# Kernel optimization log

Hardware: AMD Instinct MI355X
Metric: run time of the kernel (lower is better)

## Reference

```python
import jax, jax.numpy as jnp
import numpy as np

L = 3          # num_legs
D = 32         # leg_dim == out_leg_dim (output_dim = input_dim = D**L)
NUM_NODES = 6  # num_levels * (num_legs - 1) = 3 * 2
B = 256        # batch


def setup_inputs() -> dict:
    key = jax.random.key(0)
    k1, k2 = jax.random.split(key, 2)
    inputs = jax.random.normal(k1, (B, D ** L), dtype=jnp.float32)
    # all 6 entangler nodes share shape (D,D,D,D) since leg_dim == out_leg_dim;
    # scale ~ 1/D to mimic glorot and keep the 6-contraction chain numerically sane
    nodes = jax.random.normal(k2, (NUM_NODES, D, D, D, D), dtype=jnp.float32) / D
    bias = jnp.zeros((D ** L,), dtype=jnp.float32)
    return {"inputs": inputs, "nodes": nodes, "bias": bias}


def reference(inputs, nodes, bias):
    # Faithful port of DenseEntangler.call: reshape the input vector to L legs,
    # then contract NUM_NODES 4-leg tensors; node i eats edge slots (i%L, (i+1)%L)
    # with its axes (0,1) and replaces them with its axes (2,3).
    # jnp.tensordot output axis order (free axes of x in order, then node axes 2,3)
    # matches tn.contract_between's default ordering, so the final flatten is identical.
    Bn = inputs.shape[0]
    x = inputs.reshape((Bn,) + (D,) * L)   # axis 0 = batch, axes 1..L = legs
    pos = list(range(1, L + 1))            # edge slot k -> current axis of x
    for i in range(NUM_NODES):
        s0, s1 = i % L, (i + 1) % L
        p, q = pos[s0], pos[s1]
        x = jnp.tensordot(x, nodes[i], axes=[[p, q], [0, 1]])
        # remaining axes of x keep order (batch stays axis 0); new node axes go last
        new_pos = [0] * L
        for k in range(L):
            if k == s0:
                new_pos[k] = L - 1
            elif k == s1:
                new_pos[k] = L
            else:
                a = pos[k]
                new_pos[k] = a - (p < a) - (q < a)
        pos = new_pos
    out = x.reshape(Bn, -1) + bias  # flatten in current axis order, as in the TF code
    return jax.nn.relu(out)
```

## Files before the change

### kernel.cpp

```cpp
#include <hip/hip_runtime.h>
#include <hip/hip_bf16.h>
#include <stdint.h>

using bf16 = __hip_bfloat16;
typedef __attribute__((ext_vector_type(8))) short short8;
typedef __attribute__((ext_vector_type(4))) float floatx4;

#define DD 32
#define DL3 32768
#define BATCH 256
#define NK 1024

#define BM 256
#define BN 128
#define NKT 16
#define A_ELEM 16384
#define B_ELEM 8192
#define BUF_ELEM 24576
#define LDS_BYTES 147456

__device__ __forceinline__ void load16(const void* g, void* l) {
  __builtin_amdgcn_global_load_lds((const __attribute__((address_space(1))) void*)g,
                                   (__attribute__((address_space(3))) void*)l,
                                   16, 0, 0);
}

__global__ __launch_bounds__(256) void prep_x(const float* __restrict__ x, bf16* __restrict__ dst) {
  int b = blockIdx.x >> 5, v = blockIdx.x & 31;
  __shared__ float tile[32][33];
  const float* xb = x + (size_t)b * DL3 + v * DD;
  int t = threadIdx.x;
#pragma unroll
  for (int it = 0; it < 4; ++it) {
    int u = (t >> 5) + it * 8, f = t & 31;
    tile[u][f] = xb[u * NK + f];
  }
  __syncthreads();
  bf16* db = dst + (size_t)b * DL3 + v * NK;
#pragma unroll
  for (int it = 0; it < 4; ++it) {
    int f = (t >> 5) + it * 8, u = t & 31;
    db[f * DD + u] = __float2bfloat16(tile[u][f]);
  }
}

__global__ __launch_bounds__(256) void prep_nodes(const float* __restrict__ nodes, bf16* __restrict__ dst) {
  int id = blockIdx.x;
  int nb = id & 31, kb = (id >> 5) & 31, i = id >> 10;
  const float* src = nodes + (size_t)i * 1048576;
  bf16* d = dst + (size_t)i * 1048576;
  __shared__ float tile[32][33];
  int t = threadIdx.x;
#pragma unroll
  for (int it = 0; it < 4; ++it) {
    int u = (t >> 5) + it * 8, j = t & 31;
    tile[u][j] = src[(size_t)(u * 32 + kb) * 1024 + nb * 32 + j];
  }
  __syncthreads();
#pragma unroll
  for (int it = 0; it < 4; ++it) {
    int j = (t >> 5) + it * 8, u = t & 31;
    d[(size_t)(nb * 32 + j) * 1024 + kb * 32 + u] = __float2bfloat16(tile[u][j]);
  }
}

template <bool FINAL>
__global__ __launch_bounds__(512, 2) void entangler_gemm(
    const bf16* __restrict__ A, const bf16* __restrict__ Bn,
    bf16* __restrict__ Cb, float* __restrict__ Cf, const float* __restrict__ bias) {
  extern __shared__ char smem[];
  bf16* lds = (bf16*)smem;

  const int t = threadIdx.x;
  const int lane = t & 63;
  const int lane16 = lane & 15, quad = lane >> 4;
  const int w = t >> 6;
  const int wm = (w >> 2) & 1, wn = (w >> 1) & 1, wk = w & 1;
  const int sel = (lane16 >> 1) & 3;
  const int qs = (quad ^ sel) * 8;
  const int b0 = blockIdx.x * 8;
  const int N0 = blockIdx.y * 128;

  const int aRd = wk * 8192 + (wm * 128 + lane16) * 32 + qs;
  const int bRd = A_ELEM + wk * 4096 + (wn * 64 + lane16) * 32 + qs;

  int aOff[4], aLds[4], bOff[2], bLds[2];
#pragma unroll
  for (int r = 0; r < 4; ++r) {
    int P = (r * 512 + t) * 16;
    int L = P ^ (((P >> 7) & 3) << 4);
    int kk = L >> 14, m = (L >> 6) & 255, u0 = (L & 63) >> 1;
    aOff[r] = (b0 + (m >> 5)) * DL3 + kk * NK + (m & 31) * 32 + u0;
    aLds[r] = P >> 1;
  }
#pragma unroll
  for (int r = 0; r < 2; ++r) {
    int P = (r * 512 + t) * 16;
    int L = P ^ (((P >> 7) & 3) << 4);
    int kk = L >> 13, n = (L >> 6) & 127, u0 = (L & 63) >> 1;
    bOff[r] = (N0 + n) * NK + kk * 32 + u0;
    bLds[r] = A_ELEM + (P >> 1);
  }

  floatx4 acc[8][4];
#pragma unroll
  for (int i = 0; i < 8; ++i)
#pragma unroll
    for (int j = 0; j < 4; ++j)
      acc[i][j] = (floatx4){0.f, 0.f, 0.f, 0.f};

#pragma unroll
  for (int s = 0; s < 2; ++s) {
    bf16* bp = lds + s * BUF_ELEM;
#pragma unroll
    for (int r = 0; r < 4; ++r) load16(A + aOff[r] + s * 2048, bp + aLds[r]);
#pragma unroll
    for (int r = 0; r < 2; ++r) load16(Bn + bOff[r] + s * 64, bp + bLds[r]);
  }
  asm volatile("s_waitcnt vmcnt(6)" ::: "memory");
  __builtin_amdgcn_s_barrier();
  asm volatile("" ::: "memory");

#pragma unroll
  for (int kt = 0; kt < NKT; ++kt) {
    const bf16* bp = lds + (kt % 3) * BUF_ELEM;
    short8 af[8], bfr[4];
#pragma unroll
    for (int i = 0; i < 8; ++i) af[i] = *(const short8*)(bp + aRd + i * 512);
#pragma unroll
    for (int j = 0; j < 4; ++j) bfr[j] = *(const short8*)(bp + bRd + j * 512);
    if (kt < NKT - 2) {
      bf16* np = lds + ((kt + 2) % 3) * BUF_ELEM;
#pragma unroll
      for (int r = 0; r < 4; ++r) load16(A + aOff[r] + (kt + 2) * 2048, np + aLds[r]);
#pragma unroll
      for (int r = 0; r < 2; ++r) load16(Bn + bOff[r] + (kt + 2) * 64, np + bLds[r]);
    }
    asm volatile("" ::: "memory");
    __builtin_amdgcn_s_barrier();
    asm volatile("" ::: "memory");
    __builtin_amdgcn_s_setprio(1);
#pragma unroll
    for (int i = 0; i < 8; ++i)
#pragma unroll
      for (int j = 0; j < 4; ++j)
        acc[i][j] = __builtin_amdgcn_mfma_f32_16x16x32_bf16(af[i], bfr[j], acc[i][j], 0, 0, 0);
    __builtin_amdgcn_s_setprio(0);
    if (kt < NKT - 2) {
      asm volatile("s_waitcnt vmcnt(6)" ::: "memory");
    } else if (kt == NKT - 2) {
      asm volatile("s_waitcnt vmcnt(0)" ::: "memory");
    }
    if (kt < NKT - 1) {
      __builtin_amdgcn_s_barrier();
      asm volatile("" ::: "memory");
    }
  }

  __syncthreads();
  float* red = (float*)smem;
  const int pair = (wm << 1) | wn;
  if (wk == 1) {
    float* dst = red + pair * 8192;
#pragma unroll
    for (int i = 0; i < 8; ++i)
#pragma unroll
      for (int j = 0; j < 4; ++j)
        *(floatx4*)(dst + ((i * 4 + j) * 64 + lane) * 4) = acc[i][j];
  }
  __syncthreads();
  if (wk == 0) {
    const float* src = red + pair * 8192;
    const int R0 = blockIdx.x * 256;
#pragma unroll
    for (int i = 0; i < 8; ++i) {
#pragma unroll
      for (int j = 0; j < 4; ++j) {
        floatx4 p = *(const floatx4*)(src + ((i * 4 + j) * 64 + lane) * 4);
        acc[i][j] += p;
#pragma unroll
        for (int r = 0; r < 4; ++r) {
          int row = R0 + wm * 128 + i * 16 + quad * 4 + r;
          int col = N0 + wn * 64 + j * 16 + lane16;
          if (FINAL) {
            float v = acc[i][j][r] + bias[(row & 31) * 1024 + col];
            Cf[(size_t)row * 1024 + col] = fmaxf(v, 0.f);
          } else {
            Cb[(size_t)row * 1024 + col] = __float2bfloat16(acc[i][j][r]);
          }
        }
      }
    }
  }
}

extern "C" void kernel_launch(void* const* d_in, const int* in_sizes, int n_in,
                              void* d_out, int out_size, void* d_ws, size_t ws_size,
                              hipStream_t stream) {
  const float* x     = (const float*)d_in[0];
  const float* nodes = (const float*)d_in[1];
  const float* bias  = (const float*)d_in[2];
  float* out = (float*)d_out;

  bf16* buf0  = (bf16*)d_ws;
  bf16* buf1  = buf0 + (size_t)BATCH * DL3;
  bf16* nodeT = buf1 + (size_t)BATCH * DL3;

  static bool attr_done = false;
  if (!attr_done) {
    hipFuncSetAttribute((const void*)entangler_gemm<false>,
                        hipFuncAttributeMaxDynamicSharedMemorySize, LDS_BYTES);
    hipFuncSetAttribute((const void*)entangler_gemm<true>,
                        hipFuncAttributeMaxDynamicSharedMemorySize, LDS_BYTES);
    attr_done = true;
  }

  prep_x<<<dim3(BATCH * 32), dim3(256), 0, stream>>>(x, buf0);
  prep_nodes<<<dim3(6 * 1024), dim3(256), 0, stream>>>(nodes, nodeT);

  dim3 grid(32, 8), blk(512);
  entangler_gemm<false><<<grid, blk, LDS_BYTES, stream>>>(buf0, nodeT + (size_t)0 * 1048576, buf1, nullptr, nullptr);
  entangler_gemm<false><<<grid, blk, LDS_BYTES, stream>>>(buf1, nodeT + (size_t)1 * 1048576, buf0, nullptr, nullptr);
  entangler_gemm<false><<<grid, blk, LDS_BYTES, stream>>>(buf0, nodeT + (size_t)2 * 1048576, buf1, nullptr, nullptr);
  entangler_gemm<false><<<grid, blk, LDS_BYTES, stream>>>(buf1, nodeT + (size_t)3 * 1048576, buf0, nullptr, nullptr);
  entangler_gemm<false><<<grid, blk, LDS_BYTES, stream>>>(buf0, nodeT + (size_t)4 * 1048576, buf1, nullptr, nullptr);
  entangler_gemm<true ><<<grid, blk, LDS_BYTES, stream>>>(buf1, nodeT + (size_t)5 * 1048576, nullptr, out, bias);
}
```

Before: 231.2 us.

## Fuse six entangler GEMM launches into one cooperative kernel with grid sync

Replaces the six back-to-back GEMM launches with a single cooperative kernel that loops over the six contraction stages and uses grid.sync between them. This removes per-launch overhead and the tail/ramp gaps between kernels. The K loop is also changed from full unroll to rotating LDS buffer pointers with unroll 1, which shrinks code size but may cost some scheduling freedom. The six-launch path is kept as a fallback if the cooperative launch fails.

```diff
diff --git a/kernel.cpp b/kernel.cpp
--- a/kernel.cpp
+++ b/kernel.cpp
@@ -1,6 +1,9 @@
 #include <hip/hip_runtime.h>
+#include <hip/hip_cooperative_groups.h>
 #include <hip/hip_bf16.h>
 #include <stdint.h>
+
+namespace cg = cooperative_groups;
 
 using bf16 = __hip_bfloat16;
 typedef __attribute__((ext_vector_type(8))) short short8;
@@ -11,11 +14,8 @@
 #define BATCH 256
 #define NK 1024
 
-#define BM 256
-#define BN 128
 #define NKT 16
 #define A_ELEM 16384
-#define B_ELEM 8192
 #define BUF_ELEM 24576
 #define LDS_BYTES 147456
 
@@ -64,13 +64,157 @@
   }
 }
 
+
+__global__ __launch_bounds__(512, 2) void entangler_chain(
+    bf16* __restrict__ buf0, const bf16* __restrict__ nodeT,
+    bf16* __restrict__ buf1, float* __restrict__ out, const float* __restrict__ bias) {
+  extern __shared__ char smem[];
+  bf16* lds = (bf16*)smem;
+
+  const int t = threadIdx.x;
+  const int lane = t & 63;
+  const int lane16 = lane & 15, quad = lane >> 4;
+  const int w = t >> 6;
+  const int wm = (w >> 2) & 1, wn = (w >> 1) & 1, wk = w & 1;
+  const int sel = (lane16 >> 1) & 3;
+  const int qs = (quad ^ sel) * 8;
+  const int xt = blockIdx.x & 31, yt = blockIdx.x >> 5;
+  const int b0 = xt * 8;
+  const int N0 = yt * 128;
+
+  const int aRd = wk * 8192 + (wm * 128 + lane16) * 32 + qs;
+  const int bRd = A_ELEM + wk * 4096 + (wn * 64 + lane16) * 32 + qs;
+
+  int aOff[4], aLds[4], bOff[2], bLds[2];
+#pragma unroll
+  for (int r = 0; r < 4; ++r) {
+    int P = (r * 512 + t) * 16;
+    int L = P ^ (((P >> 7) & 3) << 4);
+    int kk = L >> 14, m = (L >> 6) & 255, u0 = (L & 63) >> 1;
+    aOff[r] = (b0 + (m >> 5)) * DL3 + kk * NK + (m & 31) * 32 + u0;
+    aLds[r] = P >> 1;
+  }
+#pragma unroll
+  for (int r = 0; r < 2; ++r) {
+    int P = (r * 512 + t) * 16;
+    int L = P ^ (((P >> 7) & 3) << 4);
+    int kk = L >> 13, n = (L >> 6) & 127, u0 = (L & 63) >> 1;
+    bOff[r] = (N0 + n) * NK + kk * 32 + u0;
+    bLds[r] = A_ELEM + (P >> 1);
+  }
+
+  cg::grid_group grid = cg::this_grid();
+
+#pragma unroll 1
+  for (int s = 0; s < 6; ++s) {
+    const bf16* Ain = (s & 1) ? buf1 : buf0;
+    bf16* Cw = (s & 1) ? buf0 : buf1;
+    const bf16* Bs = nodeT + (size_t)s * 1048576;
+    const bool FIN = (s == 5);
+
+    floatx4 acc[8][4];
+#pragma unroll
+    for (int i = 0; i < 8; ++i)
+#pragma unroll
+      for (int j = 0; j < 4; ++j)
+        acc[i][j] = (floatx4){0.f, 0.f, 0.f, 0.f};
+
+    bf16* pCur = lds;
+    bf16* pNxt = lds + BUF_ELEM;
+    bf16* pThd = lds + 2 * BUF_ELEM;
+
+#pragma unroll
+    for (int r = 0; r < 4; ++r) load16(Ain + aOff[r], pCur + aLds[r]);
+#pragma unroll
+    for (int r = 0; r < 2; ++r) load16(Bs + bOff[r], pCur + bLds[r]);
+#pragma unroll
+    for (int r = 0; r < 4; ++r) load16(Ain + aOff[r] + 2048, pNxt + aLds[r]);
+#pragma unroll
+    for (int r = 0; r < 2; ++r) load16(Bs + bOff[r] + 64, pNxt + bLds[r]);
+    asm volatile("s_waitcnt vmcnt(6)" ::: "memory");
+    __builtin_amdgcn_s_barrier();
+    asm volatile("" ::: "memory");
+
+#pragma unroll 1
+    for (int kt = 0; kt < NKT; ++kt) {
+      short8 af[8], bfr[4];
+#pragma unroll
+      for (int i = 0; i < 8; ++i) af[i] = *(const short8*)(pCur + aRd + i * 512);
+#pragma unroll
+      for (int j = 0; j < 4; ++j) bfr[j] = *(const short8*)(pCur + bRd + j * 512);
+      if (kt < NKT - 2) {
+#pragma unroll
+        for (int r = 0; r < 4; ++r) load16(Ain + aOff[r] + (kt + 2) * 2048, pThd + aLds[r]);
+#pragma unroll
+        for (int r = 0; r < 2; ++r) load16(Bs + bOff[r] + (kt + 2) * 64, pThd + bLds[r]);
+      }
+      asm volatile("" ::: "memory");
+      __builtin_amdgcn_s_barrier();
+      asm volatile("" ::: "memory");
+      __builtin_amdgcn_s_setprio(1);
+#pragma unroll
+      for (int i = 0; i < 8; ++i)
+#pragma unroll
+        for (int j = 0; j < 4; ++j)
+          acc[i][j] = __builtin_amdgcn_mfma_f32_16x16x32_bf16(af[i], bfr[j], acc[i][j], 0, 0, 0);
+      __builtin_amdgcn_s_setprio(0);
+      if (kt < NKT - 2) {
+        asm volatile("s_waitcnt vmcnt(6)" ::: "memory");
+      } else if (kt == NKT - 2) {
+        asm volatile("s_waitcnt vmcnt(0)" ::: "memory");
+      }
+      if (kt < NKT - 1) {
+        __builtin_amdgcn_s_barrier();
+        asm volatile("" ::: "memory");
+      }
+      bf16* tmp = pCur; pCur = pNxt; pNxt = pThd; pThd = tmp;
+    }
+
+    __syncthreads();
+    float* red = (float*)smem;
+    const int pair = (wm << 1) | wn;
+    if (wk == 1) {
+      float* dst = red + pair * 8192;
+#pragma unroll
+      for (int i = 0; i < 8; ++i)
+#pragma unroll
+        for (int j = 0; j < 4; ++j)
+          *(floatx4*)(dst + ((i * 4 + j) * 64 + lane) * 4) = acc[i][j];
+    }
+    __syncthreads();
+    if (wk == 0) {
+      const float* src = red + pair * 8192;
+      const int R0 = xt * 256;
+#pragma unroll
+      for (int i = 0; i < 8; ++i) {
+#pragma unroll
+        for (int j = 0; j < 4; ++j) {
+          floatx4 p = *(const floatx4*)(src + ((i * 4 + j) * 64 + lane) * 4);
+          acc[i][j] += p;
+#pragma unroll
+          for (int r = 0; r < 4; ++r) {
+            int row = R0 + wm * 128 + i * 16 + quad * 4 + r;
+            int col = N0 + wn * 64 + j * 16 + lane16;
+            if (FIN) {
+              float v = acc[i][j][r] + bias[(row & 31) * 1024 + col];
+              out[(size_t)row * 1024 + col] = fmaxf(v, 0.f);
+            } else {
+              Cw[(size_t)row * 1024 + col] = __float2bfloat16(acc[i][j][r]);
+            }
+          }
+        }
+      }
+    }
+    if (s < 5) grid.sync();
+  }
+}
+
 template <bool FINAL>
 __global__ __launch_bounds__(512, 2) void entangler_gemm(
     const bf16* __restrict__ A, const bf16* __restrict__ Bn,
     bf16* __restrict__ Cb, float* __restrict__ Cf, const float* __restrict__ bias) {
   extern __shared__ char smem[];
   bf16* lds = (bf16*)smem;
-
   const int t = threadIdx.x;
   const int lane = t & 63;
   const int lane16 = lane & 15, quad = lane >> 4;
@@ -80,10 +224,8 @@
   const int qs = (quad ^ sel) * 8;
   const int b0 = blockIdx.x * 8;
   const int N0 = blockIdx.y * 128;
-
   const int aRd = wk * 8192 + (wm * 128 + lane16) * 32 + qs;
   const int bRd = A_ELEM + wk * 4096 + (wn * 64 + lane16) * 32 + qs;
-
   int aOff[4], aLds[4], bOff[2], bLds[2];
 #pragma unroll
   for (int r = 0; r < 4; ++r) {
@@ -101,40 +243,36 @@
     bOff[r] = (N0 + n) * NK + kk * 32 + u0;
     bLds[r] = A_ELEM + (P >> 1);
   }
-
   floatx4 acc[8][4];
 #pragma unroll
   for (int i = 0; i < 8; ++i)
 #pragma unroll
     for (int j = 0; j < 4; ++j)
       acc[i][j] = (floatx4){0.f, 0.f, 0.f, 0.f};
-
-#pragma unroll
-  for (int s = 0; s < 2; ++s) {
-    bf16* bp = lds + s * BUF_ELEM;
-#pragma unroll
-    for (int r = 0; r < 4; ++r) load16(A + aOff[r] + s * 2048, bp + aLds[r]);
-#pragma unroll
-    for (int r = 0; r < 2; ++r) load16(Bn + bOff[r] + s * 64, bp + bLds[r]);
-  }
+  bf16* pCur = lds; bf16* pNxt = lds + BUF_ELEM; bf16* pThd = lds + 2 * BUF_ELEM;
+#pragma unroll
+  for (int r = 0; r < 4; ++r) load16(A + aOff[r], pCur + aLds[r]);
+#pragma unroll
+  for (int r = 0; r < 2; ++r) load16(Bn + bOff[r], pCur + bLds[r]);
+#pragma unroll
+  for (int r = 0; r < 4; ++r) load16(A + aOff[r] + 2048, pNxt + aLds[r]);
+#pragma unroll
+  for (int r = 0; r < 2; ++r) load16(Bn + bOff[r] + 64, pNxt + bLds[r]);
   asm volatile("s_waitcnt vmcnt(6)" ::: "memory");
   __builtin_amdgcn_s_barrier();
   asm volatile("" ::: "memory");
-
-#pragma unroll
+#pragma unroll 1
   for (int kt = 0; kt < NKT; ++kt) {
-    const bf16* bp = lds + (kt % 3) * BUF_ELEM;
     short8 af[8], bfr[4];
 #pragma unroll
-    for (int i = 0; i < 8; ++i) af[i] = *(const short8*)(bp + aRd + i * 512);
-#pragma unroll
-    for (int j = 0; j < 4; ++j) bfr[j] = *(const short8*)(bp + bRd + j * 512);
+    for (int i = 0; i < 8; ++i) af[i] = *(const short8*)(pCur + aRd + i * 512);
+#pragma unroll
+    for (int j = 0; j < 4; ++j) bfr[j] = *(const short8*)(pCur + bRd + j * 512);
     if (kt < NKT - 2) {
-      bf16* np = lds + ((kt + 2) % 3) * BUF_ELEM;
-#pragma unroll
-      for (int r = 0; r < 4; ++r) load16(A + aOff[r] + (kt + 2) * 2048, np + aLds[r]);
-#pragma unroll
-      for (int r = 0; r < 2; ++r) load16(Bn + bOff[r] + (kt + 2) * 64, np + bLds[r]);
+#pragma unroll
+      for (int r = 0; r < 4; ++r) load16(A + aOff[r] + (kt + 2) * 2048, pThd + aLds[r]);
+#pragma unroll
+      for (int r = 0; r < 2; ++r) load16(Bn + bOff[r] + (kt + 2) * 64, pThd + bLds[r]);
     }
     asm volatile("" ::: "memory");
     __builtin_amdgcn_s_barrier();
@@ -155,8 +293,8 @@
       __builtin_amdgcn_s_barrier();
       asm volatile("" ::: "memory");
     }
-  }
-
+    bf16* tmp = pCur; pCur = pNxt; pNxt = pThd; pThd = tmp;
+  }
   __syncthreads();
   float* red = (float*)smem;
   const int pair = (wm << 1) | wn;
@@ -208,6 +346,8 @@
 
   static bool attr_done = false;
   if (!attr_done) {
+    hipFuncSetAttribute((const void*)entangler_chain,
+                        hipFuncAttributeMaxDynamicSharedMemorySize, LDS_BYTES);
     hipFuncSetAttribute((const void*)entangler_gemm<false>,
                         hipFuncAttributeMaxDynamicSharedMemorySize, LDS_BYTES);
     hipFuncSetAttribute((const void*)entangler_gemm<true>,
@@ -218,11 +358,19 @@
   prep_x<<<dim3(BATCH * 32), dim3(256), 0, stream>>>(x, buf0);
   prep_nodes<<<dim3(6 * 1024), dim3(256), 0, stream>>>(nodes, nodeT);
 
-  dim3 grid(32, 8), blk(512);
-  entangler_gemm<false><<<grid, blk, LDS_BYTES, stream>>>(buf0, nodeT + (size_t)0 * 1048576, buf1, nullptr, nullptr);
-  entangler_gemm<false><<<grid, blk, LDS_BYTES, stream>>>(buf1, nodeT + (size_t)1 * 1048576, buf0, nullptr, nullptr);
-  entangler_gemm<false><<<grid, blk, LDS_BYTES, stream>>>(buf0, nodeT + (size_t)2 * 1048576, buf1, nullptr, nullptr);
-  entangler_gemm<false><<<grid, blk, LDS_BYTES, stream>>>(buf1, nodeT + (size_t)3 * 1048576, buf0, nullptr, nullptr);
-  entangler_gemm<false><<<grid, blk, LDS_BYTES, stream>>>(buf0, nodeT + (size_t)4 * 1048576, buf1, nullptr, nullptr);
-  entangler_gemm<true ><<<grid, blk, LDS_BYTES, stream>>>(buf1, nodeT + (size_t)5 * 1048576, nullptr, out, bias);
-}
+  bf16* a_buf0 = buf0; const bf16* a_nodeT = nodeT; bf16* a_buf1 = buf1;
+  float* a_out = out; const float* a_bias = bias;
+  void* args[] = {&a_buf0, &a_nodeT, &a_buf1, &a_out, &a_bias};
+  hipError_t e = hipLaunchCooperativeKernel((const void*)entangler_chain,
+                                            dim3(256), dim3(512), args,
+                                            LDS_BYTES, stream);
+  if (e != hipSuccess) {
+    dim3 grid(32, 8), blk(512);
+    entangler_gemm<false><<<grid, blk, LDS_BYTES, stream>>>(buf0, nodeT + (size_t)0 * 1048576, buf1, nullptr, nullptr);
+    entangler_gemm<false><<<grid, blk, LDS_BYTES, stream>>>(buf1, nodeT + (size_t)1 * 1048576, buf0, nullptr, nullptr);
+    entangler_gemm<false><<<grid, blk, LDS_BYTES, stream>>>(buf0, nodeT + (size_t)2 * 1048576, buf1, nullptr, nullptr);
+    entangler_gemm<false><<<grid, blk, LDS_BYTES, stream>>>(buf1, nodeT + (size_t)3 * 1048576, buf0, nullptr, nullptr);
+    entangler_gemm<false><<<grid, blk, LDS_BYTES, stream>>>(buf0, nodeT + (size_t)4 * 1048576, buf1, nullptr, nullptr);
+    entangler_gemm<true ><<<grid, blk, LDS_BYTES, stream>>>(buf1, nodeT + (size_t)5 * 1048576, nullptr, out, bias);
+  }
+}
```

New measurement: 526.5 us. 2.28x slower.
